# Performance work log

Measured on AMD Instinct MI355X. Metric: run time of the kernel, lower is better.

## Reference

```python
import jax, jax.numpy as jnp
import numpy as np

N_NODES, N_EDGES, N_GRAPHS, D = 32768, 49152, 1024, 64


def setup_inputs() -> dict:
    key = jax.random.key(0)
    ks = jax.random.split(key, 24)
    p = lambda k, shape, s=0.1: jax.random.normal(k, shape, dtype=jnp.float32) * s
    return dict(
        x=jax.random.normal(ks[0], (N_NODES, 14), dtype=jnp.float32),
        edge_index=jax.random.randint(ks[1], (2, N_EDGES), 0, N_NODES),
        edge_attr=jax.random.uniform(ks[2], (N_EDGES, 4), dtype=jnp.float32),
        batch=jnp.sort(jax.random.randint(ks[3], (N_NODES,), 0, N_GRAPHS)),
        lin0_W=p(ks[4], (D, 14)), lin0_b=p(ks[5], (D,)),
        e1_W=p(ks[6], (128, 4)), e1_b=p(ks[7], (128,)),
        e2_W=p(ks[8], (D * D, 128), 0.02), e2_b=p(ks[9], (D * D,), 0.02),
        root_W=p(ks[10], (D, D)), conv_b=p(ks[11], (D,)),
        gru_Wih=p(ks[12], (3 * D, D)), gru_Whh=p(ks[13], (3 * D, D)),
        gru_bih=p(ks[14], (3 * D,)), gru_bhh=p(ks[15], (3 * D,)),
        lstm_Wih=p(ks[16], (4 * D, 2 * D)), lstm_Whh=p(ks[17], (4 * D, D)),
        lstm_bih=p(ks[18], (4 * D,)), lstm_bhh=p(ks[19], (4 * D,)),
        fc1_W=p(ks[20], (128, 2 * D)), fc1_b=p(ks[21], (128,)),
        fc2_W=p(ks[22], (1, 128)), fc2_b=p(ks[23], (1,)),
    )


def reference(x, edge_index, edge_attr, batch,
              lin0_W, lin0_b, e1_W, e1_b, e2_W, e2_b, root_W, conv_b,
              gru_Wih, gru_Whh, gru_bih, gru_bhh,
              lstm_Wih, lstm_Whh, lstm_bih, lstm_bhh,
              fc1_W, fc1_b, fc2_W, fc2_b):
    N, B = x.shape[0], N_GRAPHS
    src, dst = edge_index[0], edge_index[1]

    out = jax.nn.relu(x @ lin0_W.T + lin0_b)            # [N, D]
    h = out                                             # GRU hidden (num_layers=1)

    # Edge-conditioned weights: edge_attr is constant across the 3 iterations,
    # so compute the edge MLP once (identical math to re-running it).
    W = jax.nn.relu(edge_attr @ e1_W.T + e1_b) @ e2_W.T + e2_b
    W = W.reshape(-1, D, D)                             # [E, D, D]
    cnt = jnp.maximum(
        jax.ops.segment_sum(jnp.ones((src.shape[0],), x.dtype), dst, num_segments=N), 1.0)

    for _ in range(3):
        # NNConv (aggr='mean'): gather -> per-edge matmul -> scatter-mean -> root + bias
        msg = jnp.einsum('ei,eio->eo', out[src], W)     # [E, D]
        agg = jax.ops.segment_sum(msg, dst, num_segments=N) / cnt[:, None]
        m = jax.nn.relu(agg + out @ root_W + conv_b)
        # GRU cell (seq_len=1)
        gi = m @ gru_Wih.T + gru_bih
        gh = h @ gru_Whh.T + gru_bhh
        ir, iz, inn = jnp.split(gi, 3, -1)
        hr, hz, hn = jnp.split(gh, 3, -1)
        r = jax.nn.sigmoid(ir + hr)
        z = jax.nn.sigmoid(iz + hz)
        n = jnp.tanh(inn + r * hn)
        h = (1.0 - z) * n + z * h
        out = h

    # Set2Set pooling, 3 processing steps, LSTM(2D -> D)
    q_star = jnp.zeros((B, 2 * D), x.dtype)
    hl = jnp.zeros((B, D), x.dtype)
    cl = jnp.zeros((B, D), x.dtype)
    for _ in range(3):
        g = q_star @ lstm_Wih.T + lstm_bih + hl @ lstm_Whh.T + lstm_bhh
        i_, f_, g_, o_ = jnp.split(g, 4, -1)
        cl = jax.nn.sigmoid(f_) * cl + jax.nn.sigmoid(i_) * jnp.tanh(g_)
        hl = jax.nn.sigmoid(o_) * jnp.tanh(cl)
        q = hl                                          # [B, D]
        e = jnp.sum(out * q[batch], -1)                 # [N]
        mx = jax.ops.segment_max(e, batch, num_segments=B)
        ex = jnp.exp(e - mx[batch])
        den = jax.ops.segment_sum(ex, batch, num_segments=B)
        a = ex / den[batch]                             # segment softmax
        r_read = jax.ops.segment_sum(a[:, None] * out, batch, num_segments=B)
        q_star = jnp.concatenate([q, r_read], -1)       # [B, 2D]

    hid = jax.nn.relu(q_star @ fc1_W.T + fc1_b)
    return hid @ fc2_W.T + fc2_b                        # [B, 1]
```

## Files before the change

### kernel.cpp

```cpp
#include <hip/hip_runtime.h>
#include <math.h>

#define NN_ 32768
#define NE_ 49152
#define NG_ 1024

typedef short bh8 __attribute__((ext_vector_type(8)));
typedef float f32x4 __attribute__((ext_vector_type(4)));

__device__ __forceinline__ unsigned short f2bfu(float f) {
    union { float f; unsigned int i; } x; x.f = f;
    unsigned int u = x.i;
    u += 0x7FFFu + ((u >> 16) & 1u);
    return (unsigned short)(u >> 16);
}
__device__ __forceinline__ float sigm(float x) { return 1.f / (1.f + expf(-x)); }

__global__ void MPNN_78632261256134_kernel() {}

__global__ void k_init(int* deg, float* agg) {
    int i = blockIdx.x * 256 + threadIdx.x;
    if (i < NN_) deg[i] = 0;
    int k = i - NN_;
    if (k >= 0 && k < NN_ * 64) agg[k] = 0.f;
}

__global__ void k_lin0(const float* x, const float* W, const float* b, float* node) {
    int g = blockIdx.x * 256 + threadIdx.x;
    int n = g >> 6, d = g & 63;
    const float* xr = x + n * 14;
    const float* wr = W + d * 14;
    float acc = b[d];
    for (int i = 0; i < 14; i++) acc += xr[i] * wr[i];
    node[g] = fmaxf(acc, 0.f);
}

__global__ void k_cnt(const int* dst, int* deg) {
    int e = blockIdx.x * 256 + threadIdx.x;
    if (e < NE_) atomicAdd(&deg[dst[e]], 1);
}

__global__ __launch_bounds__(256) void k_scanA(const int* __restrict__ deg,
                                               int* __restrict__ offs,
                                               int* __restrict__ bsum) {
    __shared__ int wtot[4];
    int tid = threadIdx.x, bid = blockIdx.x;
    int i = bid * 256 + tid;
    int v = deg[i];
    int sc = v;
    for (int o = 1; o < 64; o <<= 1) { int u = __shfl_up(sc, o); if ((tid & 63) >= o) sc += u; }
    if ((tid & 63) == 63) wtot[tid >> 6] = sc;
    __syncthreads();
    int wpre = 0;
    for (int k = 0; k < (tid >> 6); k++) wpre += wtot[k];
    offs[i] = sc + wpre - v;
    if (tid == 255) bsum[bid] = sc + wpre;
}

__global__ __launch_bounds__(256) void k_scanC(const int* __restrict__ bsum,
                                               int* __restrict__ offs,
                                               int* __restrict__ head) {
    __shared__ int boff;
    int tid = threadIdx.x, bid = blockIdx.x;
    if (tid == 0) {
        int s = 0;
        for (int k = 0; k < bid; k++) s += bsum[k];
        boff = s;
    }
    __syncthreads();
    int i = bid * 256 + tid;
    int o = offs[i] + boff;
    offs[i] = o; head[i] = o;
    if (i == NN_ - 1) offs[NN_] = NE_;
}

__global__ void k_scatter(const int* __restrict__ dst, int* __restrict__ head,
                          int* __restrict__ perm) {
    int e = blockIdx.x * 256 + threadIdx.x;
    if (e < NE_) { int p = atomicAdd(&head[dst[e]], 1); perm[p] = e; }
}

__global__ void k_gbnd(const int* __restrict__ batch, int* __restrict__ gb) {
    int n = blockIdx.x * 256 + threadIdx.x;
    if (n >= NN_) return;
    int b = batch[n];
    if (n == 0) { for (int g = 0; g <= b; g++) gb[g] = 0; }
    else {
        int pb = batch[n - 1];
        for (int g = pb + 1; g <= b; g++) gb[g] = n;
    }
    if (n == NN_ - 1) { for (int g = b + 1; g <= NG_; g++) gb[g] = NN_; }
}

__global__ void k_tw(const float* lWih, const float* lWhh, float* WihT2, float* WhhT2,
                     const float* fc1W, float* fc1WT) {
    int t = blockIdx.x * 256 + threadIdx.x;
    if (t < 32768) {
        int r = t >> 7, cc = t & 127; WihT2[cc * 256 + r] = lWih[t];
    } else if (t < 49152) {
        int u = t - 32768; int r = u >> 6, cc = u & 63; WhhT2[cc * 256 + r] = lWhh[u];
    } else if (t < 65536) {
        int u = t - 49152; int r = u >> 7, cc = u & 127; fc1WT[cc * 128 + r] = fc1W[u];
    }
}

__global__ void k_wfrag(const float* __restrict__ gWih, const float* __restrict__ gWhh,
                        const float* __restrict__ rootW,
                        unsigned short* __restrict__ HHh, unsigned short* __restrict__ HHl,
                        unsigned short* __restrict__ IHh, unsigned short* __restrict__ IHl) {
    int idx = blockIdx.x * 256 + threadIdx.x;
    if (idx >= 28672) return;
    float w;
    unsigned short *oh, *ol;
    if (idx < 16384) {
        int f = idx;
        int tile = f >> 9, within = f & 511;
        int l = within >> 3, j = within & 7;
        int ot = tile >> 1, kt = tile & 1;
        int col = ot * 16 + (l & 15);
        int k = kt * 32 + (l >> 4) * 8 + j;
        w = (col < 192) ? gWhh[col * 64 + k] : rootW[k * 64 + (col - 192)];
        oh = HHh + f; ol = HHl + f;
    } else {
        int f = idx - 16384;
        int tile = f >> 9, within = f & 511;
        int l = within >> 3, j = within & 7;
        int ot = tile >> 1, kt = tile & 1;
        int col = ot * 16 + (l & 15);
        int k = kt * 32 + (l >> 4) * 8 + j;
        w = gWih[col * 64 + k];
        oh = IHh + f; ol = IHl + f;
    }
    unsigned short hi = f2bfu(w);
    union { unsigned int i; float f; } hv; hv.i = (unsigned int)hi << 16;
    unsigned short lo = f2bfu(w - hv.f);
    *oh = hi; *ol = lo;
}

__global__ void k_bhat3(const float* e2W, unsigned short* Bhat3) {
    int idx = blockIdx.x * 256 + threadIdx.x;
    if (idx >= 64 * 4 * 4 * 64 * 8) return;
    int j = idx & 7, lane = (idx >> 3) & 63, t = (idx >> 9) & 3, w = (idx >> 11) & 3, s = idx >> 13;
    int row = s * 64 + w * 16 + (lane & 15);
    int k = t * 32 + (lane >> 4) * 8 + j;
    Bhat3[idx] = f2bfu(e2W[row * 128 + k]);
}

__global__ __launch_bounds__(256) void k_he(const float* __restrict__ ea,
                                            const float* __restrict__ e1W,
                                            const float* __restrict__ e1b,
                                            const int* __restrict__ perm,
                                            unsigned short* __restrict__ Hhat) {
    int tid = threadIdx.x;
    int lane = tid & 63, sub = tid >> 6;
    int gi = blockIdx.x * 4 + sub;
    int etile = gi >> 2, t = gi & 3;
    int e = etile * 16 + (lane & 15), quad = lane >> 4;
    int eo = perm[e];
    const float* ar = ea + (size_t)eo * 4;
    float a0 = ar[0], a1 = ar[1], a2 = ar[2], a3 = ar[3];
    union { unsigned short u[8]; uint4 q; } o;
#pragma unroll
    for (int j = 0; j < 8; j++) {
        int c = t * 32 + quad * 8 + j;
        const float* wr = e1W + c * 4;
        float h = e1b[c] + a0 * wr[0] + a1 * wr[1] + a2 * wr[2] + a3 * wr[3];
        o.u[j] = f2bfu(fmaxf(h, 0.f));
    }
    *(uint4*)(Hhat + (size_t)gi * 512 + lane * 8) = o.q;
}

#define PS(S) (((S) + soff) & 63)

#define LDB(B, S) {                                                                       \
        const unsigned short* _p = Bhat3 + (size_t)PS(S) * 8192 + w * 2048 + lane * 8;    \
        (B)[0] = *(const bh8*)(const void*)(_p);                                          \
        (B)[1] = *(const bh8*)(const void*)(_p + 512);                                    \
        (B)[2] = *(const bh8*)(const void*)(_p + 1024);                                   \
        (B)[3] = *(const bh8*)(const void*)(_p + 1536); }

#define LDXV(XV, S) {                                                                     \
        int sp_ = PS(S);                                                                  \
        _Pragma("unroll")                                                                 \
        for (int mt_ = 0; mt_ < 4; mt_++)                                                 \
            (XV)[mt_] = *(const f32x4*)(const void*)(xs + sp_ * 68 + mt_ * 16 + quad * 4); }

#define LDBB(BB, S) (BB) = e2b[PS(S) * 64 + w * 16 + mrow];

#define MFMA16(ACC, B) {                                                                  \
        __builtin_amdgcn_s_setprio(1);                                                    \
        _Pragma("unroll")                                                                 \
        for (int t_ = 0; t_ < 4; t_++) {                                                  \
            _Pragma("unroll")                                                             \
            for (int mt_ = 0; mt_ < 4; mt_++)                                             \
                (ACC)[mt_] = __builtin_amdgcn_mfma_f32_16x16x32_bf16(                     \
                    af[mt_][t_], (B)[t_], (t_ == 0) ? z4 : (ACC)[mt_], 0, 0, 0);          \
        }                                                                                 \
        __builtin_amdgcn_s_setprio(0); }

#define CONSUME(ACC, XV, BB) {                                                            \
        _Pragma("unroll")                                                                 \
        for (int mt_ = 0; mt_ < 4; mt_++) {                                               \
            _Pragma("unroll")                                                             \
            for (int r_ = 0; r_ < 4; r_++)                                                \
                msgv[mt_][r_] += (XV)[mt_][r_] * ((ACC)[mt_][r_] + (BB));                 \
        } }

__global__ __launch_bounds__(256, 2) void k_convr(const float* __restrict__ node,
                                                  const unsigned short* __restrict__ Hhat,
                                                  const unsigned short* __restrict__ Bhat3,
                                                  const float* __restrict__ e2b,
                                                  const int* __restrict__ src,
                                                  const int* __restrict__ dst,
                                                  const int* __restrict__ perm,
                                                  float* __restrict__ agg) {
    __shared__ __align__(16) float xs[64 * 68];
    __shared__ int dst_s[64];

    const int tid = threadIdx.x;
    const int eb = blockIdx.x * 64;
    const int lane = tid & 63, w = tid >> 6;
    const int quad = lane >> 4, mrow = lane & 15;
    const int soff = (blockIdx.x * 37) & 63;

    {
        int r = tid >> 2, c = tid & 3;
        int s = src[perm[eb + r]];
        const float* nr = node + (size_t)s * 64 + c * 16;
#pragma unroll
        for (int j = 0; j < 16; j++) xs[(c * 16 + j) * 68 + r] = nr[j];
        if (tid < 64) dst_s[tid] = dst[perm[eb + tid]];
    }

    bh8 af[4][4];
#pragma unroll
    for (int mt = 0; mt < 4; mt++)
#pragma unroll
        for (int t = 0; t < 4; t++)
            af[mt][t] = *(const bh8*)(const void*)(
                Hhat + (size_t)(((eb >> 4) + mt) * 4 + t) * 512 + lane * 8);
    __syncthreads();

    const f32x4 z4 = {0.f, 0.f, 0.f, 0.f};
    f32x4 msgv[4];
#pragma unroll
    for (int mt = 0; mt < 4; mt++) msgv[mt] = z4;

    bh8 b0[4], b1[4];
    f32x4 xvA[4], xvB[4];
    f32x4 accA[4], accB[4];
    float bbA, bbB;

    LDB(b0, 0)
    LDB(b1, 1)
    LDXV(xvA, 0)
    LDBB(bbA, 0)
    MFMA16(accA, b0)
    LDB(b0, 2)

#pragma unroll 1
    for (int s = 0; s < 62; s += 2) {
        MFMA16(accB, b1)
        LDB(b1, s + 3)
        LDXV(xvB, s + 1)
        LDBB(bbB, s + 1)
        CONSUME(accA, xvA, bbA)
        MFMA16(accA, b0)
        LDB(b0, (s + 4) & 63)
        LDXV(xvA, s + 2)
        LDBB(bbA, s + 2)
        CONSUME(accB, xvB, bbB)
    }
    MFMA16(accB, b1)
    CONSUME(accA, xvA, bbA)
    LDXV(xvB, 63)
    LDBB(bbB, 63)
    CONSUME(accB, xvB, bbB)

    __syncthreads();
#pragma unroll
    for (int mt = 0; mt < 4; mt++)
#pragma unroll
        for (int r = 0; r < 4; r++)
            xs[(mt * 16 + quad * 4 + r) * 68 + w * 16 + mrow] = msgv[mt][r];
    __syncthreads();
    {
        const int ebase = w * 16;
        const int d = lane;
        float acc = 0.f;
        int startE = ebase;
        int curn = dst_s[ebase];
#pragma unroll
        for (int e = ebase; e < ebase + 16; e++) {
            acc += xs[e * 68 + d];
            int nxt = (e < ebase + 15) ? dst_s[e + 1] : -1;
            if (nxt != curn) {
                float* dp = agg + (size_t)curn * 64 + d;
                if (startE == ebase || e == ebase + 15) atomicAdd(dp, acc);
                else *dp = acc;
                acc = 0.f; startE = e + 1; curn = nxt;
            }
        }
    }
}

__global__ __launch_bounds__(256) void k_mgru(float* __restrict__ agg,
                                              const int* __restrict__ offs,
                                              const float* __restrict__ node,
                                              const unsigned short* __restrict__ HHh,
                                              const unsigned short* __restrict__ HHl,
                                              const unsigned short* __restrict__ IHh,
                                              const unsigned short* __restrict__ IHl,
                                              const float* __restrict__ convb,
                                              const float* __restrict__ bih,
                                              const float* __restrict__ bhh,
                                              float* __restrict__ hOut) {
    __shared__ __align__(16) float hs[64][68];
    __shared__ __align__(16) float ms[64][68];
    const int tid = threadIdx.x;
    const int lane = tid & 63, wvt = tid >> 6;
    const int quad = lane >> 4, c = lane & 15;
    const int nb = blockIdx.x * 64;
    const f32x4 z4 = {0.f, 0.f, 0.f, 0.f};

    {
        int n = tid >> 2, dc = (tid & 3) * 16;
        const float* nr = node + (size_t)(nb + n) * 64 + dc;
#pragma unroll
        for (int j4 = 0; j4 < 4; j4++)
            *(f32x4*)&hs[n][dc + j4 * 4] = *(const f32x4*)(nr + j4 * 4);
    }
    __syncthreads();

    bh8 ah[2], al[2];
#pragma unroll
    for (int kt = 0; kt < 2; kt++) {
#pragma unroll
        for (int j = 0; j < 8; j++) {
            float x = hs[wvt * 16 + c][kt * 32 + quad * 8 + j];
            unsigned short h = f2bfu(x);
            union { unsigned int i; float f; } hv; hv.i = (unsigned int)h << 16;
            unsigned short l = f2bfu(x - hv.f);
            ah[kt][j] = (short)h; al[kt][j] = (short)l;
        }
    }

    f32x4 hacc[16];
#pragma unroll
    for (int ot = 0; ot < 16; ot++) {
        f32x4 a = z4;
#pragma unroll
        for (int kt = 0; kt < 2; kt++) {
            bh8 bh = *(const bh8*)(const void*)(HHh + (ot * 2 + kt) * 512 + lane * 8);
            bh8 bl = *(const bh8*)(const void*)(HHl + (ot * 2 + kt) * 512 + lane * 8);
            a = __builtin_amdgcn_mfma_f32_16x16x32_bf16(ah[kt], bh, a, 0, 0, 0);
            a = __builtin_amdgcn_mfma_f32_16x16x32_bf16(ah[kt], bl, a, 0, 0, 0);
            a = __builtin_amdgcn_mfma_f32_16x16x32_bf16(al[kt], bh, a, 0, 0, 0);
        }
        hacc[ot] = a;
    }

    int nrow[4]; float invd[4];
#pragma unroll
    for (int r = 0; r < 4; r++) {
        nrow[r] = nb + wvt * 16 + quad * 4 + r;
        int dg = offs[nrow[r] + 1] - offs[nrow[r]];
        invd[r] = 1.f / fmaxf((float)dg, 1.f);
    }
#pragma unroll
    for (int k = 0; k < 4; k++) {
        float cb = convb[c + 16 * k];
#pragma unroll
        for (int r = 0; r < 4; r++) {
            size_t ai = (size_t)nrow[r] * 64 + c + 16 * k;
            float m = fmaxf(agg[ai] * invd[r] + cb + hacc[12 + k][r], 0.f);
            agg[ai] = 0.f;
            ms[wvt * 16 + quad * 4 + r][c + 16 * k] = m;
        }
    }
    __syncthreads();

    bh8 amh[2], aml[2];
#pragma unroll
    for (int kt = 0; kt < 2; kt++) {
#pragma unroll
        for (int j = 0; j < 8; j++) {
            float x = ms[wvt * 16 + c][kt * 32 + quad * 8 + j];
            unsigned short h = f2bfu(x);
            union { unsigned int i; float f; } hv; hv.i = (unsigned int)h << 16;
            unsigned short l = f2bfu(x - hv.f);
            amh[kt][j] = (short)h; aml[kt][j] = (short)l;
        }
    }

    f32x4 macc[12];
#pragma unroll
    for (int ot = 0; ot < 12; ot++) {
        f32x4 a = z4;
#pragma unroll
        for (int kt = 0; kt < 2; kt++) {
            bh8 bh = *(const bh8*)(const void*)(IHh + (ot * 2 + kt) * 512 + lane * 8);
            bh8 bl = *(const bh8*)(const void*)(IHl + (ot * 2 + kt) * 512 + lane * 8);
            a = __builtin_amdgcn_mfma_f32_16x16x32_bf16(amh[kt], bh, a, 0, 0, 0);
            a = __builtin_amdgcn_mfma_f32_16x16x32_bf16(amh[kt], bl, a, 0, 0, 0);
            a = __builtin_amdgcn_mfma_f32_16x16x32_bf16(aml[kt], bh, a, 0, 0, 0);
        }
        macc[ot] = a;
    }

#pragma unroll
    for (int k = 0; k < 4; k++) {
        int d = c + 16 * k;
        float bir = bih[d], biz = bih[64 + d], bin = bih[128 + d];
        float bhr = bhh[d], bhz = bhh[64 + d], bhn = bhh[128 + d];
#pragma unroll
        for (int r = 0; r < 4; r++) {
            float rr = sigm(macc[k][r] + bir + hacc[k][r] + bhr);
            float zz = sigm(macc[4 + k][r] + biz + hacc[4 + k][r] + bhz);
            float hnv = hacc[8 + k][r] + bhn;
            float nn = tanhf(macc[8 + k][r] + bin + rr * hnv);
            float hold = hs[wvt * 16 + quad * 4 + r][d];
            hOut[(size_t)nrow[r] * 64 + d] = (1.f - zz) * nn + zz * hold;
        }
    }
}

__global__ __launch_bounds__(256) void k_s2s3(const float* __restrict__ node,
                                              const int* __restrict__ gb,
                                              const float* __restrict__ WihT2,
                                              const float* __restrict__ WhhT2,
                                              const float* __restrict__ bih,
                                              const float* __restrict__ bhh,
                                              float* __restrict__ qstar) {
    __shared__ float qvs[128];
    __shared__ float hls[64], cls[64], qsh[64];
    __shared__ float accs[4][64];
    __shared__ float es[256];
    __shared__ float red[4][64];
    __shared__ float sred[4];
    const int b = blockIdx.x, tid = threadIdx.x;
    const int lane = tid & 63, wv = tid >> 6;
    const int start = gb[b], end = gb[b + 1];

    if (tid < 128) qvs[tid] = 0.f;
    else if (tid < 192) hls[tid - 128] = 0.f;
    else cls[tid - 192] = 0.f;
    __syncthreads();

    for (int step = 0; step < 3; step++) {
        float acc = bih[wv * 64 + lane] + bhh[wv * 64 + lane];
        if (step > 0) {
            const float* wih = WihT2 + wv * 64 + lane;
            const float* whh = WhhT2 + wv * 64 + lane;
#pragma unroll 4
            for (int j = 0; j < 128; j++) acc += qvs[j] * wih[(size_t)j * 256];
#pragma unroll 4
            for (int j = 0; j < 64; j++) acc += hls[j] * whh[(size_t)j * 256];
        }
        accs[wv][lane] = acc;
        __syncthreads();
        if (tid < 64) {
            float c = sigm(accs[1][tid]) * cls[tid] + sigm(accs[0][tid]) * tanhf(accs[2][tid]);
            cls[tid] = c;
            float q = sigm(accs[3][tid]) * tanhf(c);
            hls[tid] = q; qsh[tid] = q;
        }
        __syncthreads();
        const float q = qsh[lane];

        float m_run = -1e30f, l_run = 0.f, r_part = 0.f;
        for (int cbase = start; cbase < end; cbase += 256) {
            int cn = min(256, end - cbase);
            for (int i = wv; i < cn; i += 4) {
                float nv = node[(size_t)(cbase + i) * 64 + lane];
                float p = nv * q;
#pragma unroll
                for (int o = 32; o > 0; o >>= 1) p += __shfl_xor(p, o);
                if (lane == 0) es[i] = p;
            }
            __syncthreads();
            float mloc = -1e30f;
            for (int i = tid; i < cn; i += 256) mloc = fmaxf(mloc, es[i]);
#pragma unroll
            for (int o = 32; o > 0; o >>= 1) mloc = fmaxf(mloc, __shfl_xor(mloc, o));
            if (lane == 0) sred[wv] = mloc;
            __syncthreads();
            float m_chunk = fmaxf(fmaxf(sred[0], sred[1]), fmaxf(sred[2], sred[3]));
            float m_new = fmaxf(m_run, m_chunk);
            float sc = expf(m_run - m_new);
            float lloc = 0.f;
            for (int i = tid; i < cn; i += 256) {
                float wgt = expf(es[i] - m_new);
                es[i] = wgt; lloc += wgt;
            }
#pragma unroll
            for (int o = 32; o > 0; o >>= 1) lloc += __shfl_xor(lloc, o);
            __syncthreads();
            if (lane == 0) sred[wv] = lloc;
            __syncthreads();
            float l_chunk = sred[0] + sred[1] + sred[2] + sred[3];
            l_run = l_run * sc + l_chunk;
            r_part *= sc;
            for (int i = wv; i < cn; i += 4)
                r_part += es[i] * node[(size_t)(cbase + i) * 64 + lane];
            m_run = m_new;
            __syncthreads();
        }
        red[wv][lane] = r_part;
        __syncthreads();
        if (tid < 64) {
            float r = red[0][tid] + red[1][tid] + red[2][tid] + red[3][tid];
            qvs[tid] = qsh[tid];
            qvs[64 + tid] = (end > start) ? r / l_run : 0.f;
        }
        __syncthreads();
    }
    if (tid < 128) qstar[(size_t)b * 128 + tid] = qvs[tid];
}

__global__ void k_fc(const float* qstar, const float* W1T, const float* b1,
                     const float* W2, const float* b2, float* out) {
    __shared__ float hid[128];
    __shared__ float qs[128];
    int b = blockIdx.x; int t = threadIdx.x;
    qs[t] = qstar[(size_t)b * 128 + t];
    __syncthreads();
    float acc = b1[t];
    for (int k = 0; k < 128; k++) acc += qs[k] * W1T[k * 128 + t];
    hid[t] = fmaxf(acc, 0.f);
    __syncthreads();
    if (t < 64) {
        float s = hid[t] * W2[t] + hid[t + 64] * W2[t + 64];
        for (int o = 32; o > 0; o >>= 1) s += __shfl_xor(s, o);
        if (t == 0) out[b] = s + b2[0];
    }
}

extern "C" void kernel_launch(void* const* d_in, const int* in_sizes, int n_in,
                              void* d_out, int out_size, void* d_ws, size_t ws_size,
                              hipStream_t stream) {
    const float* x     = (const float*)d_in[0];
    const int*   ei    = (const int*)d_in[1];
    const float* ea    = (const float*)d_in[2];
    const int*   batch = (const int*)d_in[3];
    const float* lin0W = (const float*)d_in[4];
    const float* lin0b = (const float*)d_in[5];
    const float* e1W   = (const float*)d_in[6];
    const float* e1b   = (const float*)d_in[7];
    const float* e2W   = (const float*)d_in[8];
    const float* e2b   = (const float*)d_in[9];
    const float* rootW = (const float*)d_in[10];
    const float* convb = (const float*)d_in[11];
    const float* gWih  = (const float*)d_in[12];
    const float* gWhh  = (const float*)d_in[13];
    const float* gbih  = (const float*)d_in[14];
    const float* gbhh  = (const float*)d_in[15];
    const float* lWih  = (const float*)d_in[16];
    const float* lWhh  = (const float*)d_in[17];
    const float* lbih  = (const float*)d_in[18];
    const float* lbhh  = (const float*)d_in[19];
    const float* fc1W  = (const float*)d_in[20];
    const float* fc1b  = (const float*)d_in[21];
    const float* fc2W  = (const float*)d_in[22];
    const float* fc2b  = (const float*)d_in[23];
    const int* src = ei;
    const int* dst = ei + NE_;

    char* p = (char*)d_ws;
    auto alloc = [&](size_t bytes) -> char* {
        char* r = p; p += (bytes + 255) & ~(size_t)255; return r;
    };
    unsigned short* Bhat3 = (unsigned short*)alloc((size_t)524288 * 2);
    unsigned short* Hhat  = (unsigned short*)alloc((size_t)NE_ * 128 * 2);
    float* nodeA  = (float*)alloc((size_t)NN_ * 64 * 4);
    float* nodeB  = (float*)alloc((size_t)NN_ * 64 * 4);
    float* aggb   = (float*)alloc((size_t)NN_ * 64 * 4);
    int*   deg    = (int*)alloc((size_t)NN_ * 4);
    int*   offs   = (int*)alloc((size_t)(NN_ + 1) * 4);
    int*   head   = (int*)alloc((size_t)NN_ * 4);
    int*   perm   = (int*)alloc((size_t)NE_ * 4);
    int*   bsum   = (int*)alloc((size_t)128 * 4);
    int*   gb     = (int*)alloc((size_t)(NG_ + 1) * 4);
    unsigned short* HHh = (unsigned short*)alloc((size_t)16384 * 2);
    unsigned short* HHl = (unsigned short*)alloc((size_t)16384 * 2);
    unsigned short* IHh = (unsigned short*)alloc((size_t)12288 * 2);
    unsigned short* IHl = (unsigned short*)alloc((size_t)12288 * 2);
    float* WihT2  = (float*)alloc(256 * 128 * 4);
    float* WhhT2  = (float*)alloc(256 * 64 * 4);
    float* fc1WT  = (float*)alloc(128 * 128 * 4);
    float* qstar  = (float*)alloc((size_t)NG_ * 128 * 4);

    k_init<<<(NN_ + NN_ * 64 + 255) / 256, 256, 0, stream>>>(deg, aggb);
    k_lin0<<<NN_ * 64 / 256, 256, 0, stream>>>(x, lin0W, lin0b, nodeA);
    k_cnt<<<NE_ / 256, 256, 0, stream>>>(dst, deg);
    k_scanA<<<NN_ / 256, 256, 0, stream>>>(deg, offs, bsum);
    k_scanC<<<NN_ / 256, 256, 0, stream>>>(bsum, offs, head);
    k_scatter<<<NE_ / 256, 256, 0, stream>>>(dst, head, perm);
    k_gbnd<<<NN_ / 256, 256, 0, stream>>>(batch, gb);
    k_tw<<<256, 256, 0, stream>>>(lWih, lWhh, WihT2, WhhT2, fc1W, fc1WT);
    k_wfrag<<<112, 256, 0, stream>>>(gWih, gWhh, rootW, HHh, HHl, IHh, IHl);
    k_bhat3<<<524288 / 256, 256, 0, stream>>>(e2W, Bhat3);
    k_he<<<NE_ / 16, 256, 0, stream>>>(ea, e1W, e1b, perm, Hhat);

    float* curF = nodeA; float* nxtF = nodeB;
    for (int it = 0; it < 3; it++) {
        k_convr<<<NE_ / 64, 256, 0, stream>>>(curF, Hhat, Bhat3, e2b, src, dst, perm, aggb);
        k_mgru<<<NN_ / 64, 256, 0, stream>>>(aggb, offs, curF, HHh, HHl, IHh, IHl,
                                             convb, gbih, gbhh, nxtF);
        float* tf = curF; curF = nxtF; nxtF = tf;
    }

    k_s2s3<<<NG_, 256, 0, stream>>>(curF, gb, WihT2, WhhT2, lbih, lbhh, qstar);
    k_fc<<<NG_, 128, 0, stream>>>(qstar, fc1WT, fc1b, fc2W, fc2b, (float*)d_out);
}
```

Baseline: 425.2 us.

## Retile edge-conv kernel to 192-edge blocks with 2D wave split

The per-edge NNConv kernel now processes 192 edges per block with 512 threads, instead of 64 edges with 256 threads. The 8 waves form a 4x2 grid: each wave covers 48 edges and 32 output columns, computing a 3x2 tile of MFMA accumulators per step. The goal is one block per CU across the grid, removing the partial last wave of blocks, and more independent MFMAs per step. In exchange, the shared B fragments are reloaded once per 48 edges rather than once per 64. The previous xv/bias software prefetch is replaced by a simpler double-buffered B load with inline LDS reads.

```diff
diff --git a/kernel.cpp b/kernel.cpp
--- a/kernel.cpp
+++ b/kernel.cpp
@@ -172,131 +172,147 @@
 
 #define PS(S) (((S) + soff) & 63)
 
-#define LDB(B, S) {                                                                       \
-        const unsigned short* _p = Bhat3 + (size_t)PS(S) * 8192 + w * 2048 + lane * 8;    \
-        (B)[0] = *(const bh8*)(const void*)(_p);                                          \
-        (B)[1] = *(const bh8*)(const void*)(_p + 512);                                    \
-        (B)[2] = *(const bh8*)(const void*)(_p + 1024);                                   \
-        (B)[3] = *(const bh8*)(const void*)(_p + 1536); }
-
-#define LDXV(XV, S) {                                                                     \
-        int sp_ = PS(S);                                                                  \
+#define LDB8(B, S) {                                                                      \
+        const unsigned short* _p = Bhat3 + (size_t)PS(S) * 8192 + (w2 * 2) * 2048 + lane * 8; \
         _Pragma("unroll")                                                                 \
-        for (int mt_ = 0; mt_ < 4; mt_++)                                                 \
-            (XV)[mt_] = *(const f32x4*)(const void*)(xs + sp_ * 68 + mt_ * 16 + quad * 4); }
-
-#define LDBB(BB, S) (BB) = e2b[PS(S) * 64 + w * 16 + mrow];
-
-#define MFMA16(ACC, B) {                                                                  \
-        __builtin_amdgcn_s_setprio(1);                                                    \
-        _Pragma("unroll")                                                                 \
-        for (int t_ = 0; t_ < 4; t_++) {                                                  \
+        for (int j_ = 0; j_ < 2; j_++)                                                    \
             _Pragma("unroll")                                                             \
-            for (int mt_ = 0; mt_ < 4; mt_++)                                             \
-                (ACC)[mt_] = __builtin_amdgcn_mfma_f32_16x16x32_bf16(                     \
-                    af[mt_][t_], (B)[t_], (t_ == 0) ? z4 : (ACC)[mt_], 0, 0, 0);          \
-        }                                                                                 \
-        __builtin_amdgcn_s_setprio(0); }
-
-#define CONSUME(ACC, XV, BB) {                                                            \
-        _Pragma("unroll")                                                                 \
-        for (int mt_ = 0; mt_ < 4; mt_++) {                                               \
-            _Pragma("unroll")                                                             \
-            for (int r_ = 0; r_ < 4; r_++)                                                \
-                msgv[mt_][r_] += (XV)[mt_][r_] * ((ACC)[mt_][r_] + (BB));                 \
-        } }
-
-__global__ __launch_bounds__(256, 2) void k_convr(const float* __restrict__ node,
-                                                  const unsigned short* __restrict__ Hhat,
-                                                  const unsigned short* __restrict__ Bhat3,
-                                                  const float* __restrict__ e2b,
-                                                  const int* __restrict__ src,
-                                                  const int* __restrict__ dst,
-                                                  const int* __restrict__ perm,
-                                                  float* __restrict__ agg) {
-    __shared__ __align__(16) float xs[64 * 68];
-    __shared__ int dst_s[64];
+            for (int t_ = 0; t_ < 4; t_++)                                                \
+                (B)[j_][t_] = *(const bh8*)(const void*)(_p + j_ * 2048 + t_ * 512); }
+
+__global__ __launch_bounds__(512) void k_convr(const float* __restrict__ node,
+                                               const unsigned short* __restrict__ Hhat,
+                                               const unsigned short* __restrict__ Bhat3,
+                                               const float* __restrict__ e2b,
+                                               const int* __restrict__ src,
+                                               const int* __restrict__ dst,
+                                               const int* __restrict__ perm,
+                                               float* __restrict__ agg) {
+    __shared__ __align__(16) float xs[64 * 204];
+    __shared__ int dst_s[192];
 
     const int tid = threadIdx.x;
-    const int eb = blockIdx.x * 64;
-    const int lane = tid & 63, w = tid >> 6;
+    const int eb = blockIdx.x * 192;
+    const int lane = tid & 63, w8 = tid >> 6;
+    const int w2 = w8 & 1, m2 = w8 >> 1;
     const int quad = lane >> 4, mrow = lane & 15;
     const int soff = (blockIdx.x * 37) & 63;
 
     {
-        int r = tid >> 2, c = tid & 3;
-        int s = src[perm[eb + r]];
-        const float* nr = node + (size_t)s * 64 + c * 16;
-#pragma unroll
-        for (int j = 0; j < 16; j++) xs[(c * 16 + j) * 68 + r] = nr[j];
-        if (tid < 64) dst_s[tid] = dst[perm[eb + tid]];
-    }
-
-    bh8 af[4][4];
-#pragma unroll
-    for (int mt = 0; mt < 4; mt++)
+#pragma unroll
+        for (int base = 0; base < 768; base += 512) {
+            int u = base + tid;
+            if (u < 768) {
+                int r = u >> 2, c = u & 3;
+                int s = src[perm[eb + r]];
+                const float* nr = node + (size_t)s * 64 + c * 16;
+#pragma unroll
+                for (int j = 0; j < 16; j++) xs[(c * 16 + j) * 204 + r] = nr[j];
+            }
+        }
+        if (tid < 192) dst_s[tid] = dst[perm[eb + tid]];
+    }
+
+    bh8 af[3][4];
+#pragma unroll
+    for (int i = 0; i < 3; i++)
 #pragma unroll
         for (int t = 0; t < 4; t++)
-            af[mt][t] = *(const bh8*)(const void*)(
-                Hhat + (size_t)(((eb >> 4) + mt) * 4 + t) * 512 + lane * 8);
+            af[i][t] = *(const bh8*)(const void*)(
+                Hhat + (size_t)(((eb >> 4) + m2 * 3 + i) * 4 + t) * 512 + lane * 8);
     __syncthreads();
 
     const f32x4 z4 = {0.f, 0.f, 0.f, 0.f};
-    f32x4 msgv[4];
-#pragma unroll
-    for (int mt = 0; mt < 4; mt++) msgv[mt] = z4;
-
-    bh8 b0[4], b1[4];
-    f32x4 xvA[4], xvB[4];
-    f32x4 accA[4], accB[4];
-    float bbA, bbB;
-
-    LDB(b0, 0)
-    LDB(b1, 1)
-    LDXV(xvA, 0)
-    LDBB(bbA, 0)
-    MFMA16(accA, b0)
-    LDB(b0, 2)
+    f32x4 msg[3][2];
+#pragma unroll
+    for (int i = 0; i < 3; i++)
+#pragma unroll
+        for (int j = 0; j < 2; j++) msg[i][j] = z4;
+
+    bh8 b0[2][4], b1[2][4];
+    LDB8(b0, 0)
 
 #pragma unroll 1
-    for (int s = 0; s < 62; s += 2) {
-        MFMA16(accB, b1)
-        LDB(b1, s + 3)
-        LDXV(xvB, s + 1)
-        LDBB(bbB, s + 1)
-        CONSUME(accA, xvA, bbA)
-        MFMA16(accA, b0)
-        LDB(b0, (s + 4) & 63)
-        LDXV(xvA, s + 2)
-        LDBB(bbA, s + 2)
-        CONSUME(accB, xvB, bbB)
-    }
-    MFMA16(accB, b1)
-    CONSUME(accA, xvA, bbA)
-    LDXV(xvB, 63)
-    LDBB(bbB, 63)
-    CONSUME(accB, xvB, bbB)
-
-    __syncthreads();
-#pragma unroll
-    for (int mt = 0; mt < 4; mt++)
-#pragma unroll
-        for (int r = 0; r < 4; r++)
-            xs[(mt * 16 + quad * 4 + r) * 68 + w * 16 + mrow] = msgv[mt][r];
+    for (int s = 0; s < 64; s += 2) {
+        if (s + 1 < 64) LDB8(b1, s + 1)
+        {
+            float bbv0 = e2b[PS(s) * 64 + (w2 * 2) * 16 + mrow];
+            float bbv1 = e2b[PS(s) * 64 + (w2 * 2 + 1) * 16 + mrow];
+            f32x4 acc[3][2];
+            __builtin_amdgcn_s_setprio(1);
+#pragma unroll
+            for (int t = 0; t < 4; t++)
+#pragma unroll
+                for (int i = 0; i < 3; i++)
+#pragma unroll
+                    for (int j = 0; j < 2; j++)
+                        acc[i][j] = __builtin_amdgcn_mfma_f32_16x16x32_bf16(
+                            af[i][t], b0[j][t], (t == 0) ? z4 : acc[i][j], 0, 0, 0);
+            __builtin_amdgcn_s_setprio(0);
+            int sp = PS(s);
+#pragma unroll
+            for (int i = 0; i < 3; i++) {
+                f32x4 xv = *(const f32x4*)(const void*)(
+                    xs + sp * 204 + (m2 * 3 + i) * 16 + quad * 4);
+#pragma unroll
+                for (int r = 0; r < 4; r++) {
+                    msg[i][0][r] += xv[r] * (acc[i][0][r] + bbv0);
+                    msg[i][1][r] += xv[r] * (acc[i][1][r] + bbv1);
+                }
+            }
+        }
+        if (s + 2 < 64) LDB8(b0, s + 2)
+        if (s + 1 < 64) {
+            float bbv0 = e2b[PS(s + 1) * 64 + (w2 * 2) * 16 + mrow];
+            float bbv1 = e2b[PS(s + 1) * 64 + (w2 * 2 + 1) * 16 + mrow];
+            f32x4 acc[3][2];
+            __builtin_amdgcn_s_setprio(1);
+#pragma unroll
+            for (int t = 0; t < 4; t++)
+#pragma unroll
+                for (int i = 0; i < 3; i++)
+#pragma unroll
+                    for (int j = 0; j < 2; j++)
+                        acc[i][j] = __builtin_amdgcn_mfma_f32_16x16x32_bf16(
+                            af[i][t], b1[j][t], (t == 0) ? z4 : acc[i][j], 0, 0, 0);
+            __builtin_amdgcn_s_setprio(0);
+            int sp = PS(s + 1);
+#pragma unroll
+            for (int i = 0; i < 3; i++) {
+                f32x4 xv = *(const f32x4*)(const void*)(
+                    xs + sp * 204 + (m2 * 3 + i) * 16 + quad * 4);
+#pragma unroll
+                for (int r = 0; r < 4; r++) {
+                    msg[i][0][r] += xv[r] * (acc[i][0][r] + bbv0);
+                    msg[i][1][r] += xv[r] * (acc[i][1][r] + bbv1);
+                }
+            }
+        }
+    }
+
+    __syncthreads();
+#pragma unroll
+    for (int i = 0; i < 3; i++)
+#pragma unroll
+        for (int j = 0; j < 2; j++)
+#pragma unroll
+            for (int r = 0; r < 4; r++)
+                xs[((m2 * 3 + i) * 16 + quad * 4 + r) * 68 + (w2 * 2 + j) * 16 + mrow]
+                    = msg[i][j][r];
     __syncthreads();
     {
-        const int ebase = w * 16;
+        const int ebase = w8 * 24;
         const int d = lane;
         float acc = 0.f;
         int startE = ebase;
         int curn = dst_s[ebase];
 #pragma unroll
-        for (int e = ebase; e < ebase + 16; e++) {
+        for (int e = ebase; e < ebase + 24; e++) {
             acc += xs[e * 68 + d];
-            int nxt = (e < ebase + 15) ? dst_s[e + 1] : -1;
+            int nxt = (e < ebase + 23) ? dst_s[e + 1] : -1;
             if (nxt != curn) {
                 float* dp = agg + (size_t)curn * 64 + d;
-                if (startE == ebase || e == ebase + 15) atomicAdd(dp, acc);
+                if (startE == ebase || e == ebase + 23) atomicAdd(dp, acc);
                 else *dp = acc;
                 acc = 0.f; startE = e + 1; curn = nxt;
             }
@@ -604,7 +620,7 @@
 
     float* curF = nodeA; float* nxtF = nodeB;
     for (int it = 0; it < 3; it++) {
-        k_convr<<<NE_ / 64, 256, 0, stream>>>(curF, Hhat, Bhat3, e2b, src, dst, perm, aggb);
+        k_convr<<<NE_ / 192, 512, 0, stream>>>(curF, Hhat, Bhat3, e2b, src, dst, perm, aggb);
         k_mgru<<<NN_ / 64, 256, 0, stream>>>(aggb, offs, curF, HHh, HHl, IHh, IHl,
                                              convb, gbih, gbhh, nxtF);
         float* tf = curF; curF = nxtF; nxtF = tf;
```

Result: no change. 432.7 us (+1.8%).
